# Performance work log

Hardware: AMD Instinct MI355X
Metric: run time of the kernel (lower is better)

Reference implementation:

```python
import jax, jax.numpy as jnp
import numpy as np

PHI = 1.618033988749895

def phi_spiral(x):
    # sigmoid(x/phi) * (x*phi / (1+|x|))
    return jax.nn.sigmoid(x / PHI) * (x * PHI / (1.0 + jnp.abs(x)))

def setup_inputs() -> dict:
    key = jax.random.key(0)
    ks = jax.random.split(key, 9)
    B, D = 262144, 256
    return {
        "x": jax.random.normal(ks[0], (B, D), dtype=jnp.float32),
        "W_in": jax.random.normal(ks[1], (49, D), dtype=jnp.float32) * 0.05,
        "b_in": jax.random.normal(ks[2], (49,), dtype=jnp.float32) * 0.05,
        "Wn": jax.random.normal(ks[3], (7, 7, 49), dtype=jnp.float32) * 0.05,
        "bn": jax.random.normal(ks[4], (7, 7), dtype=jnp.float32) * 0.05,
        "W_int": jax.random.normal(ks[5], (21, 49), dtype=jnp.float32) * 0.05,
        "b_int": jax.random.normal(ks[6], (21,), dtype=jnp.float32) * 0.05,
        "gamma": jnp.ones((21,), dtype=jnp.float32),
        "beta": jnp.zeros((21,), dtype=jnp.float32),
        "W_out": jax.random.normal(ks[7], (4, 21), dtype=jnp.float32) * 0.05,
        "b_out": jax.random.normal(ks[8], (4,), dtype=jnp.float32) * 0.05,
    }

def reference(x, W_in, b_in, Wn, bn, W_int, b_int, gamma, beta, W_out, b_out):
    # input transform + phi spiral (dropout is identity in eval)
    h = phi_spiral(x @ W_in.T + b_in)                    # [B, 49]
    # 7 parallel 49->7 linears, batched; concat order = neuron order k
    z = jnp.einsum('bi,khi->bkh', h, Wn) + bn            # [B, 7, 7]
    combined = phi_spiral(z).reshape(h.shape[0], 49)     # [B, 49]
    integrated = phi_spiral(combined @ W_int.T + b_int)  # [B, 21]
    # LayerNorm over last dim (eps=1e-5, torch default)
    mu = jnp.mean(integrated, axis=-1, keepdims=True)
    var = jnp.mean((integrated - mu) ** 2, axis=-1, keepdims=True)
    normed = (integrated - mu) * jax.lax.rsqrt(var + 1e-5) * gamma + beta
    out = normed @ W_out.T + b_out                       # [B, 4]
    return out
```

## Files before the change

kernel.cpp:

```cpp
#include <hip/hip_runtime.h>

#define PHI     1.618033988749895f
#define INV_PHI 0.6180339887498949f
#define NTILES  4

typedef _Float16 f16x8 __attribute__((ext_vector_type(8)));
typedef float    f32x4 __attribute__((ext_vector_type(4)));

typedef const __attribute__((address_space(1))) void gas_void;
typedef __attribute__((address_space(3))) void las_void;

__device__ __forceinline__ float phi_spiral(float v) {
    float e = __expf(-v * INV_PHI);
    float d = (1.0f + e) * (1.0f + fabsf(v));
    return __fdividef(v * PHI, d);
}

__device__ __forceinline__ void cp16(const void* g, void* l) {
    __builtin_amdgcn_global_load_lds((gas_void*)g, (las_void*)l, 16, 0, 0);
}

#define WS_B1 0
#define WS_B2 16384
#define WS_B3 20480
#define WS_BIAS_BYTES 65536

__global__ void prep_kernel(
    const float* __restrict__ W_in, const float* __restrict__ b_in,
    const float* __restrict__ Wn,   const float* __restrict__ bn,
    const float* __restrict__ W_int,const float* __restrict__ b_int,
    _Float16* __restrict__ wsh, float* __restrict__ wsb)
{
    if (blockIdx.x == 11) {
        const int t = threadIdx.x;
        if (t < 64)       wsb[t] = (t < 49)        ? b_in[t]        : 0.f;
        else if (t < 128) wsb[t] = (t - 64 < 49)   ? bn[t - 64]     : 0.f;
        else if (t < 160) wsb[t] = (t - 128 < 21)  ? b_int[t - 128] : 0.f;
        return;
    }
    const int g    = blockIdx.x * 256 + threadIdx.x;
    const int lane = g & 63;
    const int fid  = g >> 6;
    const int lr = lane & 15, lk = lane >> 4;
    f16x8 o;
    if (fid < 32) {
        const int ks = fid >> 2, nt = fid & 3;
        const int n = nt * 16 + lr, kb = ks * 32 + lk * 8;
#pragma unroll 8
        for (int j = 0; j < 8; ++j) {
            const int k = kb + j;
            o[j] = (_Float16)((n < 49) ? W_in[n * 256 + k] : 0.f);
        }
        *reinterpret_cast<f16x8*>(wsh + WS_B1 + (size_t)(fid * 64 + lane) * 8) = o;
    } else if (fid < 40) {
        const int f = fid - 32, ks = f >> 2, nt = f & 3;
        const int n = nt * 16 + lr, kb = ks * 32 + lk * 8;
#pragma unroll 8
        for (int j = 0; j < 8; ++j) {
            const int k = kb + j;
            o[j] = (_Float16)((n < 49 && k < 49) ? Wn[n * 49 + k] : 0.f);
        }
        *reinterpret_cast<f16x8*>(wsh + WS_B2 + (size_t)(f * 64 + lane) * 8) = o;
    } else {
        const int f = fid - 40, ks = f >> 1, nt = f & 1;
        const int n = nt * 16 + lr, kb = ks * 32 + lk * 8;
#pragma unroll 8
        for (int j = 0; j < 8; ++j) {
            const int k = kb + j;
            o[j] = (_Float16)((n < 21 && k < 49) ? W_int[n * 49 + k] : 0.f);
        }
        *reinterpret_cast<f16x8*>(wsh + WS_B3 + (size_t)(f * 64 + lane) * 8) = o;
    }
}

__global__ __launch_bounds__(1024)
__attribute__((amdgpu_waves_per_eu(4, 8)))
void seven_neurons_mfma(
    const float* __restrict__ x,
    const _Float16* __restrict__ wsh, const float* __restrict__ wsb,
    const float* __restrict__ gamma, const float* __restrict__ beta,
    const float* __restrict__ W_out, const float* __restrict__ b_out,
    float* __restrict__ out)
{
    __shared__ __align__(16) unsigned char lds[45056 + 16 * 6656];

    const int t = threadIdx.x;
    const int lane = t & 63, wv = t >> 6;
    const int lr = lane & 15, lk = lane >> 4;

    unsigned char* ldsW  = lds;
    unsigned char* xslot = lds + 45056 + wv * 6656;
    unsigned char* wslot = xslot + 4096;

    float b1v[4], b2v[4], b3v[2];
#pragma unroll 4
    for (int nt = 0; nt < 4; ++nt) { b1v[nt] = wsb[nt * 16 + lr]; b2v[nt] = wsb[64 + nt * 16 + lr]; }
#pragma unroll 2
    for (int nt = 0; nt < 2; ++nt) b3v[nt] = wsb[128 + nt * 16 + lr];

    const unsigned char* wsrc = (const unsigned char*)wsh;
#pragma unroll 1
    for (int f = wv; f < 44; f += 16)
        cp16(wsrc + (size_t)f * 1024 + lane * 16, ldsW + (size_t)f * 1024);

    const int srow = lane >> 3;
    const int sgr  = (lane & 7) ^ srow;
    const float* xsrc = x + ((size_t)blockIdx.x * NTILES * 256 + wv * 16 + srow) * 256 + sgr * 4;

    cp16(xsrc + 0,           xslot + 0);
    cp16(xsrc + 2048,        xslot + 1024);
    cp16(xsrc + 32,          xslot + 2048);
    cp16(xsrc + 32 + 2048,   xslot + 3072);

    asm volatile("s_waitcnt vmcnt(4)" ::: "memory");
    __builtin_amdgcn_sched_barrier(0);
    __builtin_amdgcn_s_barrier();

    const int xoff0 = lr * 128 + (((2 * lk)     ^ (lr & 7)) << 4);
    const int xoff1 = lr * 128 + (((2 * lk + 1) ^ (lr & 7)) << 4);

#pragma unroll 1
    for (int it = 0; it < NTILES; ++it) {
        f32x4 acc1[4];
#pragma unroll 4
        for (int ni = 0; ni < 4; ++ni) acc1[ni] = (f32x4){0.f, 0.f, 0.f, 0.f};

#pragma unroll
        for (int k = 0; k < 8; ++k) {
            if (it == NTILES - 1 && k == 7)
                asm volatile("s_waitcnt vmcnt(0)" ::: "memory");
            else
                asm volatile("s_waitcnt vmcnt(2)" ::: "memory");
            __builtin_amdgcn_sched_barrier(0);

            const unsigned char* xc = xslot + (k & 1) * 2048;
            const f32x4 r0 = *reinterpret_cast<const f32x4*>(xc + xoff0);
            const f32x4 r1 = *reinterpret_cast<const f32x4*>(xc + xoff1);
            const f16x8 a = { (_Float16)r0[0], (_Float16)r0[1], (_Float16)r0[2], (_Float16)r0[3],
                              (_Float16)r1[0], (_Float16)r1[1], (_Float16)r1[2], (_Float16)r1[3] };

            asm volatile("s_waitcnt lgkmcnt(0)" ::: "memory");
            __builtin_amdgcn_sched_barrier(0);
            const int g2 = it * 8 + k + 2;
            if (g2 < NTILES * 8) {
                const float* s0 = xsrc + (size_t)(g2 >> 3) * 65536 + (g2 & 7) * 32;
                cp16(s0,        xslot + (k & 1) * 2048);
                cp16(s0 + 2048, xslot + (k & 1) * 2048 + 1024);
            }

#pragma unroll 4
            for (int nt = 0; nt < 4; ++nt) {
                const f16x8 bf = *reinterpret_cast<const f16x8*>(
                    ldsW + (size_t)(k * 4 + nt) * 1024 + lane * 16);
                acc1[nt] = __builtin_amdgcn_mfma_f32_16x16x32_f16(a, bf, acc1[nt], 0, 0, 0);
            }
        }

        {
            _Float16* H = (_Float16*)wslot;
#pragma unroll 4
            for (int nt = 0; nt < 4; ++nt)
#pragma unroll 4
                for (int r = 0; r < 4; ++r) {
                    const int row = lk * 4 + r;
                    const float v = phi_spiral(acc1[nt][r] + b1v[nt]);
                    H[row * 72 + nt * 16 + lr] = (_Float16)v;
                }
        }

        f32x4 acc2[4];
#pragma unroll 4
        for (int ni = 0; ni < 4; ++ni) acc2[ni] = (f32x4){0.f, 0.f, 0.f, 0.f};
#pragma unroll 2
        for (int ks = 0; ks < 2; ++ks) {
            const f16x8 a = *reinterpret_cast<const f16x8*>(
                wslot + lr * 144 + (ks * 32 + lk * 8) * 2);
#pragma unroll 4
            for (int nt = 0; nt < 4; ++nt) {
                const f16x8 bf = *reinterpret_cast<const f16x8*>(
                    ldsW + 32768 + (size_t)((ks * 4 + nt) * 64 + lane) * 16);
                acc2[nt] = __builtin_amdgcn_mfma_f32_16x16x32_f16(a, bf, acc2[nt], 0, 0, 0);
            }
        }
        {
            _Float16* H = (_Float16*)wslot;
#pragma unroll 4
            for (int nt = 0; nt < 4; ++nt)
#pragma unroll 4
                for (int r = 0; r < 4; ++r) {
                    const int row = lk * 4 + r;
                    const float v = phi_spiral(acc2[nt][r] + b2v[nt]);
                    H[row * 72 + nt * 16 + lr] = (_Float16)v;
                }
        }

        f32x4 acc3[2];
#pragma unroll 2
        for (int ni = 0; ni < 2; ++ni) acc3[ni] = (f32x4){0.f, 0.f, 0.f, 0.f};
#pragma unroll 2
        for (int ks = 0; ks < 2; ++ks) {
            const f16x8 a = *reinterpret_cast<const f16x8*>(
                wslot + lr * 144 + (ks * 32 + lk * 8) * 2);
#pragma unroll 2
            for (int nt = 0; nt < 2; ++nt) {
                const f16x8 bf = *reinterpret_cast<const f16x8*>(
                    ldsW + 40960 + (size_t)((ks * 2 + nt) * 64 + lane) * 16);
                acc3[nt] = __builtin_amdgcn_mfma_f32_16x16x32_f16(a, bf, acc3[nt], 0, 0, 0);
            }
        }
        {
            float* F = (float*)wslot;
#pragma unroll 2
            for (int nt = 0; nt < 2; ++nt)
#pragma unroll 4
                for (int r = 0; r < 4; ++r) {
                    const int col = nt * 16 + lr;
                    const int row = lk * 4 + r;
                    if (col < 21)
                        F[row * 25 + col] = phi_spiral(acc3[nt][r] + b3v[nt]);
                }
        }

        {
            const int r = t >> 2, p = t & 3;
            const float* my = (const float*)(lds + 45056 + (size_t)(r >> 4) * 6656 + 4096)
                              + (r & 15) * 25;
            float v[21];
#pragma unroll 21
            for (int o = 0; o < 21; ++o) v[o] = my[o];
            float mu = 0.f;
#pragma unroll 21
            for (int o = 0; o < 21; ++o) mu += v[o];
            mu *= (1.0f / 21.0f);
            float var = 0.f;
#pragma unroll 21
            for (int o = 0; o < 21; ++o) { float d = v[o] - mu; var = fmaf(d, d, var); }
            var *= (1.0f / 21.0f);
            const float rs = rsqrtf(var + 1e-5f);
            float acc = b_out[p];
#pragma unroll 21
            for (int o = 0; o < 21; ++o)
                acc = fmaf((v[o] - mu) * rs * gamma[o] + beta[o], W_out[p * 21 + o], acc);
            out[((size_t)blockIdx.x * NTILES + it) * 1024 + t] = acc;
        }
    }
}

extern "C" void kernel_launch(void* const* d_in, const int* in_sizes, int n_in,
                              void* d_out, int out_size, void* d_ws, size_t ws_size,
                              hipStream_t stream) {
    const float* x     = (const float*)d_in[0];
    const float* W_in  = (const float*)d_in[1];
    const float* b_in  = (const float*)d_in[2];
    const float* Wn    = (const float*)d_in[3];
    const float* bn    = (const float*)d_in[4];
    const float* W_int = (const float*)d_in[5];
    const float* b_int = (const float*)d_in[6];
    const float* gamma = (const float*)d_in[7];
    const float* beta  = (const float*)d_in[8];
    const float* W_out = (const float*)d_in[9];
    const float* b_out = (const float*)d_in[10];
    float* out = (float*)d_out;

    _Float16* wsh = (_Float16*)d_ws;
    float*    wsb = (float*)((char*)d_ws + WS_BIAS_BYTES);

    prep_kernel<<<12, 256, 0, stream>>>(W_in, b_in, Wn, bn, W_int, b_int, wsh, wsb);

    const int B = in_sizes[0] / 256;
    seven_neurons_mfma<<<B / (NTILES * 256), 1024, 0, stream>>>(
        x, wsh, wsb, gamma, beta, W_out, b_out, out);
}
```

Before: 59.35 us.

## Load x tiles directly into registers with double-buffered halves instead of LDS staging

Replaces the asynchronous global-to-LDS staging of x, with its manual vmcnt waits and swizzled LDS reads, by direct per-lane global loads into two register buffers. Each buffer holds half a tile's K range and is prefetched one half ahead of the MFMA work. This removes the LDS round trip and cuts per-wave LDS use, and waves_per_eu is pinned to 4. The cost is many more live VGPRs and reliance on the compiler to overlap the loads. Each lane now reads 32-byte chunks strided across rows rather than the earlier coalesced cp16 pattern.

```diff
diff --git a/kernel.cpp b/kernel.cpp
--- a/kernel.cpp
+++ b/kernel.cpp
@@ -73,8 +73,31 @@
     }
 }
 
+#define ISSUE_HALF(DST, G) do {                                                   \
+    const float* _s = xw + (size_t)((G) >> 1) * 65536 + ((G) & 1) * 128 + lk * 8; \
+    _Pragma("unroll 4")                                                           \
+    for (int kk = 0; kk < 4; ++kk) {                                              \
+        DST[2 * kk]     = *reinterpret_cast<const f32x4*>(_s + kk * 32);          \
+        DST[2 * kk + 1] = *reinterpret_cast<const f32x4*>(_s + kk * 32 + 4);      \
+    } } while (0)
+
+#define COMPUTE_HALF(SRC, KS0) do {                                               \
+    _Pragma("unroll 4")                                                           \
+    for (int kk = 0; kk < 4; ++kk) {                                              \
+        const f16x8 a = { (_Float16)SRC[2*kk][0],   (_Float16)SRC[2*kk][1],       \
+                          (_Float16)SRC[2*kk][2],   (_Float16)SRC[2*kk][3],       \
+                          (_Float16)SRC[2*kk+1][0], (_Float16)SRC[2*kk+1][1],     \
+                          (_Float16)SRC[2*kk+1][2], (_Float16)SRC[2*kk+1][3] };   \
+        _Pragma("unroll 4")                                                       \
+        for (int nt = 0; nt < 4; ++nt) {                                          \
+            const f16x8 bf = *reinterpret_cast<const f16x8*>(                     \
+                ldsW + (size_t)(((KS0) + kk) * 4 + nt) * 1024 + lane * 16);       \
+            acc1[nt] = __builtin_amdgcn_mfma_f32_16x16x32_f16(a, bf, acc1[nt],    \
+                                                              0, 0, 0);           \
+        } } } while (0)
+
 __global__ __launch_bounds__(1024)
-__attribute__((amdgpu_waves_per_eu(4, 8)))
+__attribute__((amdgpu_waves_per_eu(4, 4)))
 void seven_neurons_mfma(
     const float* __restrict__ x,
     const _Float16* __restrict__ wsh, const float* __restrict__ wsb,
@@ -82,15 +105,14 @@
     const float* __restrict__ W_out, const float* __restrict__ b_out,
     float* __restrict__ out)
 {
-    __shared__ __align__(16) unsigned char lds[45056 + 16 * 6656];
+    __shared__ __align__(16) unsigned char lds[45056 + 16 * 2560];
 
     const int t = threadIdx.x;
     const int lane = t & 63, wv = t >> 6;
     const int lr = lane & 15, lk = lane >> 4;
 
     unsigned char* ldsW  = lds;
-    unsigned char* xslot = lds + 45056 + wv * 6656;
-    unsigned char* wslot = xslot + 4096;
+    unsigned char* wslot = lds + 45056 + wv * 2560;
 
     float b1v[4], b2v[4], b3v[2];
 #pragma unroll 4
@@ -102,22 +124,12 @@
 #pragma unroll 1
     for (int f = wv; f < 44; f += 16)
         cp16(wsrc + (size_t)f * 1024 + lane * 16, ldsW + (size_t)f * 1024);
-
-    const int srow = lane >> 3;
-    const int sgr  = (lane & 7) ^ srow;
-    const float* xsrc = x + ((size_t)blockIdx.x * NTILES * 256 + wv * 16 + srow) * 256 + sgr * 4;
-
-    cp16(xsrc + 0,           xslot + 0);
-    cp16(xsrc + 2048,        xslot + 1024);
-    cp16(xsrc + 32,          xslot + 2048);
-    cp16(xsrc + 32 + 2048,   xslot + 3072);
-
-    asm volatile("s_waitcnt vmcnt(4)" ::: "memory");
-    __builtin_amdgcn_sched_barrier(0);
-    __builtin_amdgcn_s_barrier();
-
-    const int xoff0 = lr * 128 + (((2 * lk)     ^ (lr & 7)) << 4);
-    const int xoff1 = lr * 128 + (((2 * lk + 1) ^ (lr & 7)) << 4);
+    __syncthreads();
+
+    const float* xw = x + ((size_t)blockIdx.x * NTILES * 256 + wv * 16 + lr) * 256;
+
+    f32x4 xA[8], xB[8];
+    ISSUE_HALF(xA, 0);
 
 #pragma unroll 1
     for (int it = 0; it < NTILES; ++it) {
@@ -125,36 +137,10 @@
 #pragma unroll 4
         for (int ni = 0; ni < 4; ++ni) acc1[ni] = (f32x4){0.f, 0.f, 0.f, 0.f};
 
-#pragma unroll
-        for (int k = 0; k < 8; ++k) {
-            if (it == NTILES - 1 && k == 7)
-                asm volatile("s_waitcnt vmcnt(0)" ::: "memory");
-            else
-                asm volatile("s_waitcnt vmcnt(2)" ::: "memory");
-            __builtin_amdgcn_sched_barrier(0);
-
-            const unsigned char* xc = xslot + (k & 1) * 2048;
-            const f32x4 r0 = *reinterpret_cast<const f32x4*>(xc + xoff0);
-            const f32x4 r1 = *reinterpret_cast<const f32x4*>(xc + xoff1);
-            const f16x8 a = { (_Float16)r0[0], (_Float16)r0[1], (_Float16)r0[2], (_Float16)r0[3],
-                              (_Float16)r1[0], (_Float16)r1[1], (_Float16)r1[2], (_Float16)r1[3] };
-
-            asm volatile("s_waitcnt lgkmcnt(0)" ::: "memory");
-            __builtin_amdgcn_sched_barrier(0);
-            const int g2 = it * 8 + k + 2;
-            if (g2 < NTILES * 8) {
-                const float* s0 = xsrc + (size_t)(g2 >> 3) * 65536 + (g2 & 7) * 32;
-                cp16(s0,        xslot + (k & 1) * 2048);
-                cp16(s0 + 2048, xslot + (k & 1) * 2048 + 1024);
-            }
-
-#pragma unroll 4
-            for (int nt = 0; nt < 4; ++nt) {
-                const f16x8 bf = *reinterpret_cast<const f16x8*>(
-                    ldsW + (size_t)(k * 4 + nt) * 1024 + lane * 16);
-                acc1[nt] = __builtin_amdgcn_mfma_f32_16x16x32_f16(a, bf, acc1[nt], 0, 0, 0);
-            }
-        }
+        ISSUE_HALF(xB, 2 * it + 1);
+        COMPUTE_HALF(xA, 0);
+        if (it + 1 < NTILES) ISSUE_HALF(xA, 2 * it + 2);
+        COMPUTE_HALF(xB, 4);
 
         {
             _Float16* H = (_Float16*)wslot;
@@ -223,7 +209,7 @@
 
         {
             const int r = t >> 2, p = t & 3;
-            const float* my = (const float*)(lds + 45056 + (size_t)(r >> 4) * 6656 + 4096)
+            const float* my = (const float*)(lds + 45056 + (size_t)(r >> 4) * 2560)
                               + (r & 15) * 25;
             float v[21];
 #pragma unroll 21
```

Result: slower. 69.89 us (+17.8%).
